# Optimization experiments

Hardware: AMD Instinct MI355X
Metric: run time of the kernel (lower is better)

## Reference

```python
import jax, jax.numpy as jnp
import numpy as np

EPS = 1e-12  # F.normalize eps

def _normalize(v, axis):
    n = jnp.sqrt(jnp.sum(v * v, axis=axis, keepdims=True))
    return v / jnp.maximum(n, EPS)

def setup_inputs() -> dict:
    key = jax.random.key(0)
    ks = jax.random.split(key, 7)
    N, D, E = 100000, 128, 1600000
    x = jax.random.normal(ks[0], (N, D), dtype=jnp.float32)
    edge_index = jax.random.randint(ks[1], (2, E), 0, N, dtype=jnp.int64)
    s = 1.0 / np.sqrt(D)
    W_l = jax.random.normal(ks[2], (D, D), dtype=jnp.float32) * s
    b_l = jnp.zeros((D,), dtype=jnp.float32)
    W_r = jax.random.normal(ks[3], (D, D), dtype=jnp.float32) * s
    W1 = jax.random.normal(ks[4], (D, 10), dtype=jnp.float32)
    W2 = jax.random.normal(ks[5], (D, 20), dtype=jnp.float32)
    return {"x": x, "edge_index": edge_index, "W_l": W_l, "b_l": b_l,
            "W_r": W_r, "W1": W1, "W2": W2}

def reference(x, edge_index, W_l, b_l, W_r, W1, W2):
    N = x.shape[0]
    src, dst = edge_index[0], edge_index[1]
    # SAGEConv mean aggregation: gather source feats, scatter-mean to targets
    msg = x[src]                                   # [E, D]
    agg = jax.ops.segment_sum(msg, dst, num_segments=N)     # [N, D]
    deg = jax.ops.segment_sum(jnp.ones_like(dst, dtype=x.dtype), dst,
                              num_segments=N)               # [N]
    agg = agg / jnp.maximum(deg, 1.0)[:, None]
    # out = lin_l(agg) + lin_r(x)
    h = agg @ W_l + b_l + x @ W_r                  # [N, D]
    # NormedLinear heads: 10 * norm(h, dim=1) @ norm(W, dim=0)
    hn = _normalize(h, axis=1)
    out1 = 10.0 * (hn @ _normalize(W1, axis=0))
    out2 = 10.0 * (hn @ _normalize(W2, axis=0))
    return (out1, out2, h)
```

## Files before the change

kernel.cpp:

```cpp
#include <hip/hip_runtime.h>
#include <math.h>


typedef __attribute__((ext_vector_type(8))) short s16x8;
typedef __attribute__((ext_vector_type(4))) float f32x4;

#define NBLK 128
#define BLKT 512
#define SH 8
#define BMASK 255

static __device__ __forceinline__ unsigned short f2b(float f) {
  unsigned u = __builtin_bit_cast(unsigned, f);
  u += 0x7fff + ((u >> 16) & 1);
  return (unsigned short)(u >> 16);
}
static __device__ __forceinline__ float b2f(unsigned short s) {
  unsigned u = ((unsigned)s) << 16;
  return __builtin_bit_cast(float, u);
}


__global__ __launch_bounds__(BLKT) void radix_hist(
    const int* __restrict__ ei, int* __restrict__ G, int E, int nb, int CH)
{
  __shared__ int cnt[512];
  const int b = blockIdx.x;
  const int t = threadIdx.x;
  for (int i = t; i < 512; i += BLKT) cnt[i] = 0;
  __syncthreads();
  const int e0 = b * CH, e1 = min(E, e0 + CH);
  for (int e = e0 + t; e < e1; e += BLKT)
    atomicAdd(&cnt[ei[(size_t)E + e] >> SH], 1);
  __syncthreads();
  for (int k = t; k < nb; k += BLKT)
    G[(size_t)k * NBLK + b] = cnt[k];
}

#define SCAN_CHUNK 2048

__global__ __launch_bounds__(256) void scan1_kernel(
    const int* __restrict__ cnt, int* __restrict__ offs,
    int* __restrict__ csum, int n)
{
  __shared__ int s_scan[256];
  const int t = threadIdx.x;
  const int base = blockIdx.x * SCAN_CHUNK + t * 8;
  int v[8];
  int s = 0;
#pragma unroll
  for (int k = 0; k < 8; ++k) {
    v[k] = (base + k < n) ? cnt[base + k] : 0;
    s += v[k];
  }
  s_scan[t] = s;
  __syncthreads();
#pragma unroll
  for (int off = 1; off < 256; off <<= 1) {
    int add = (t >= off) ? s_scan[t - off] : 0;
    __syncthreads();
    s_scan[t] += add;
    __syncthreads();
  }
  int run = s_scan[t] - s;
#pragma unroll
  for (int k = 0; k < 8; ++k) {
    if (base + k < n) offs[base + k] = run;
    run += v[k];
  }
  if (t == 255) csum[blockIdx.x] = s_scan[255];
}

__global__ __launch_bounds__(256) void scan2_kernel(int* __restrict__ csum, int nc)
{
  __shared__ int s_scan[256];
  const int t = threadIdx.x;
  int c = (t < nc) ? csum[t] : 0;
  s_scan[t] = c;
  __syncthreads();
#pragma unroll
  for (int off = 1; off < 256; off <<= 1) {
    int add = (t >= off) ? s_scan[t - off] : 0;
    __syncthreads();
    s_scan[t] += add;
    __syncthreads();
  }
  if (t < nc) csum[t] = s_scan[t] - c;
}

__global__ __launch_bounds__(256) void scan3_add(
    int* __restrict__ G, const int* __restrict__ csum, int n)
{
  int i = blockIdx.x * blockDim.x + threadIdx.x;
  if (i < n) G[i] += csum[i / SCAN_CHUNK];
}

__global__ __launch_bounds__(BLKT) void radix_scatter(
    const int* __restrict__ ei, const int* __restrict__ G,
    int* __restrict__ ebuf, int E, int nb, int CH)
{
  __shared__ int cur[512];
  const int b = blockIdx.x;
  const int t = threadIdx.x;
  for (int k = t; k < nb; k += BLKT) cur[k] = G[(size_t)k * NBLK + b];
  __syncthreads();
  const int e0 = b * CH, e1 = min(E, e0 + CH);
  for (int e = e0 + t; e < e1; e += BLKT) {
    int src = ei[e];
    int dst = ei[(size_t)E + e];
    int pos = atomicAdd(&cur[dst >> SH], 1);
    ebuf[pos] = (src << SH) | (dst & BMASK);
  }
}

__global__ __launch_bounds__(256) void csr_finalize(
    const int* __restrict__ G, const int* __restrict__ ebuf,
    int* __restrict__ offs, int* __restrict__ elist, int N, int E, int nb)
{
  __shared__ int cnt[256];
  __shared__ int sc[256];
  __shared__ int cur[256];
  const int b = blockIdx.x;
  const int t = threadIdx.x;
  const int e0 = G[(size_t)b * NBLK];
  const int e1 = (b + 1 < nb) ? G[(size_t)(b + 1) * NBLK] : E;

  cnt[t] = 0;
  __syncthreads();
  for (int j = e0 + t; j < e1; j += 256)
    atomicAdd(&cnt[ebuf[j] & BMASK], 1);
  __syncthreads();
  int v = cnt[t];
  sc[t] = v;
  __syncthreads();
#pragma unroll
  for (int off = 1; off < 256; off <<= 1) {
    int add = (t >= off) ? sc[t - off] : 0;
    __syncthreads();
    sc[t] += add;
    __syncthreads();
  }
  int ex = e0 + sc[t] - v;
  int node = (b << SH) + t;
  if (node < N) offs[node] = ex;
  cur[t] = ex;
  if (b == 0 && t == 0) offs[N] = E;
  __syncthreads();
  for (int j = e0 + t; j < e1; j += 256) {
    int w = ebuf[j];
    int pos = atomicAdd(&cur[w & BMASK], 1);
    elist[pos] = w >> SH;
  }
}


__global__ __launch_bounds__(256) void conv_x_kernel(
    const float* __restrict__ x, short* __restrict__ xb, int n8)
{
  int stride = gridDim.x * blockDim.x;
  for (int i = blockIdx.x * blockDim.x + threadIdx.x; i < n8; i += stride) {
    float4 v0 = ((const float4*)x)[(size_t)i * 2];
    float4 v1 = ((const float4*)x)[(size_t)i * 2 + 1];
    s16x8 o;
    o[0] = (short)f2b(v0.x); o[1] = (short)f2b(v0.y);
    o[2] = (short)f2b(v0.z); o[3] = (short)f2b(v0.w);
    o[4] = (short)f2b(v1.x); o[5] = (short)f2b(v1.y);
    o[6] = (short)f2b(v1.z); o[7] = (short)f2b(v1.w);
    ((s16x8*)xb)[i] = o;
  }
}


__global__ __launch_bounds__(256) void agg_gather_b(
    const short* __restrict__ xb, const int* __restrict__ offs,
    const int* __restrict__ elist, short* __restrict__ aggb, int N)
{
  const int lane = threadIdx.x & 63;
  const int row = blockIdx.x * 4 + (threadIdx.x >> 6);
  if (row >= N) return;
  const int qt = lane >> 4;
  const int c  = lane & 15;
  const int start = offs[row], end = offs[row + 1];
  float a[8] = {0.f, 0.f, 0.f, 0.f, 0.f, 0.f, 0.f, 0.f};
  for (int j = start + qt; j < end; j += 4) {
    const s16x8 v = *(const s16x8*)&xb[(size_t)elist[j] * 128 + c * 8];
#pragma unroll
    for (int k = 0; k < 8; ++k) a[k] += b2f((unsigned short)v[k]);
  }
#pragma unroll
  for (int k = 0; k < 8; ++k) {
    a[k] += __shfl_xor(a[k], 16);
    a[k] += __shfl_xor(a[k], 32);
  }
  if (qt == 0) {
    float rd = 1.0f / fmaxf((float)(end - start), 1.0f);
    s16x8 o;
#pragma unroll
    for (int k = 0; k < 8; ++k) o[k] = (short)f2b(a[k] * rd);
    *(s16x8*)&aggb[(size_t)row * 128 + c * 8] = o;
  }
}

__global__ __launch_bounds__(256) void conv_w_kernel(
    const float* __restrict__ Wl, const float* __restrict__ Wr,
    short* __restrict__ wbT)
{
  int i = blockIdx.x * blockDim.x + threadIdx.x;
  if (i < 128 * 256) {
    int c = i >> 8;
    int k = i & 255;
    float v = (k < 128) ? Wl[(size_t)k * 128 + c] : Wr[(size_t)(k - 128) * 128 + c];
    wbT[i] = (short)f2b(v);
  }
}


__global__ __launch_bounds__(256, 2) void gemm_mfma(
    const short* __restrict__ aggb, const float* __restrict__ x,
    const short* __restrict__ wbT, const float* __restrict__ bl,
    float* __restrict__ h, int N)
{
  __shared__ short A_s[128][72];
  __shared__ short B_s[128][72];

  const int t = threadIdx.x;
  const int lane = t & 63;
  const int wid = t >> 6;
  const int wr = wid >> 1;
  const int wc = wid & 1;
  const int row0 = blockIdx.x * 128;
  const int l15 = lane & 15;
  const int lhi = lane >> 4;

  f32x4 acc[4][4];
#pragma unroll
  for (int m = 0; m < 4; ++m)
#pragma unroll
    for (int n = 0; n < 4; ++n) acc[m][n] = (f32x4){0.f, 0.f, 0.f, 0.f};

  for (int kc = 0; kc < 4; ++kc) {
    __syncthreads();
    const int kbase = (kc & 1) * 64;
#pragma unroll
    for (int uu = 0; uu < 4; ++uu) {
      int u = t + uu * 256;
      int r = u >> 3;
      int s = u & 7;
      s16x8 va = {0, 0, 0, 0, 0, 0, 0, 0};
      int grow = row0 + r;
      if (grow < N) {
        if (kc < 2) {
          va = *(const s16x8*)&aggb[(size_t)grow * 128 + kbase + s * 8];
        } else {
          float4 f0 = ((const float4*)x)[(size_t)grow * 32 + (kc & 1) * 16 + s * 2];
          float4 f1 = ((const float4*)x)[(size_t)grow * 32 + (kc & 1) * 16 + s * 2 + 1];
          va[0] = (short)f2b(f0.x); va[1] = (short)f2b(f0.y);
          va[2] = (short)f2b(f0.z); va[3] = (short)f2b(f0.w);
          va[4] = (short)f2b(f1.x); va[5] = (short)f2b(f1.y);
          va[6] = (short)f2b(f1.z); va[7] = (short)f2b(f1.w);
        }
      }
      *(s16x8*)&A_s[r][s * 8] = va;
      s16x8 vb = *(const s16x8*)&wbT[(size_t)r * 256 + kc * 64 + s * 8];
      *(s16x8*)&B_s[r][s * 8] = vb;
    }
    __syncthreads();

#pragma unroll
    for (int ks = 0; ks < 64; ks += 32) {
      const int klo = ks + lhi * 8;
      s16x8 af[4], bf[4];
#pragma unroll
      for (int m = 0; m < 4; ++m)
        af[m] = *(const s16x8*)&A_s[wr * 64 + m * 16 + l15][klo];
#pragma unroll
      for (int n = 0; n < 4; ++n)
        bf[n] = *(const s16x8*)&B_s[wc * 64 + n * 16 + l15][klo];
#pragma unroll
      for (int m = 0; m < 4; ++m)
#pragma unroll
        for (int n = 0; n < 4; ++n)
          acc[m][n] = __builtin_amdgcn_mfma_f32_16x16x32_bf16(
              af[m], bf[n], acc[m][n], 0, 0, 0);
    }
  }

  float bcol[4];
#pragma unroll
  for (int n = 0; n < 4; ++n) bcol[n] = bl[wc * 64 + n * 16 + l15];
#pragma unroll
  for (int m = 0; m < 4; ++m) {
    int grow_base = row0 + wr * 64 + m * 16 + lhi * 4;
#pragma unroll
    for (int r = 0; r < 4; ++r) {
      int grow = grow_base + r;
      if (grow < N) {
#pragma unroll
        for (int n = 0; n < 4; ++n) {
          int col = wc * 64 + n * 16 + l15;
          h[(size_t)grow * 128 + col] = acc[m][n][r] + bcol[n];
        }
      }
    }
  }
}


__global__ __launch_bounds__(256) void edge_scatter(
    const float* __restrict__ x, const int* __restrict__ ei,
    float* __restrict__ agg, float* __restrict__ deg, int E)
{
  long long total = (long long)E * 32;
  long long stride = (long long)gridDim.x * blockDim.x;
  for (long long i = (long long)blockIdx.x * blockDim.x + threadIdx.x;
       i < total; i += stride) {
    int e = (int)(i >> 5);
    int c = (int)(i & 31);
    int src = ei[e];
    int dst = ei[(size_t)E + e];
    float4 v = ((const float4*)x)[(size_t)src * 32 + c];
    float* a = agg + (size_t)dst * 128 + c * 4;
    atomicAdd(a + 0, v.x);
    atomicAdd(a + 1, v.y);
    atomicAdd(a + 2, v.z);
    atomicAdd(a + 3, v.w);
    if (c == 0) atomicAdd(deg + dst, 1.0f);
  }
}

#define FMA4(accR, wv, s) { accR[0] += (s) * wv.x; accR[1] += (s) * wv.y; \
                            accR[2] += (s) * wv.z; accR[3] += (s) * wv.w; }

__global__ __launch_bounds__(256, 2) void gemm_h(
    const float* __restrict__ x, const float* __restrict__ Wl,
    const float* __restrict__ bl, const float* __restrict__ Wr,
    const float* __restrict__ degf, float* __restrict__ aggh, int N)
{
  __shared__ float a_s[128][36];
  __shared__ float x_s[128][36];
  __shared__ float wl_s[32][128];
  __shared__ float wr_s[32][128];

  const int t = threadIdx.x;
  const int tx = t & 15;
  const int ty = t >> 4;
  const int row0 = blockIdx.x * 128;

  float acc0[8][4];
  float acc1[8][4];
#pragma unroll
  for (int r = 0; r < 8; ++r)
#pragma unroll
    for (int c = 0; c < 4; ++c) { acc0[r][c] = 0.f; acc1[r][c] = 0.f; }

  for (int kc = 0; kc < 4; ++kc) {
    __syncthreads();
#pragma unroll
    for (int j = 0; j < 4; ++j) {
      int i = t + 256 * j;
      int r = i >> 3;
      int c4 = i & 7;
      int row = row0 + r;
      float4 av = {0.f, 0.f, 0.f, 0.f};
      float4 xv = {0.f, 0.f, 0.f, 0.f};
      if (row < N) {
        float rd = 1.0f / fmaxf(degf[row], 1.0f);
        av = ((const float4*)aggh)[(size_t)row * 32 + kc * 8 + c4];
        av.x *= rd; av.y *= rd; av.z *= rd; av.w *= rd;
        xv = ((const float4*)x)[(size_t)row * 32 + kc * 8 + c4];
      }
      *(float4*)&a_s[r][c4 * 4] = av;
      *(float4*)&x_s[r][c4 * 4] = xv;
    }
#pragma unroll
    for (int j = 0; j < 4; ++j) {
      int i = t + 256 * j;
      int kk = i >> 5;
      int c4 = i & 31;
      ((float4*)wl_s[kk])[c4] = ((const float4*)Wl)[(size_t)(kc * 32 + kk) * 32 + c4];
      ((float4*)wr_s[kk])[c4] = ((const float4*)Wr)[(size_t)(kc * 32 + kk) * 32 + c4];
    }
    __syncthreads();

#pragma unroll
    for (int k4 = 0; k4 < 8; ++k4) {
      float4 wl0[4], wl1[4], wr0[4], wr1[4];
#pragma unroll
      for (int kk = 0; kk < 4; ++kk) {
        int k = k4 * 4 + kk;
        wl0[kk] = *(const float4*)&wl_s[k][tx * 4];
        wl1[kk] = *(const float4*)&wl_s[k][64 + tx * 4];
        wr0[kk] = *(const float4*)&wr_s[k][tx * 4];
        wr1[kk] = *(const float4*)&wr_s[k][64 + tx * 4];
      }
#pragma unroll
      for (int r = 0; r < 8; ++r) {
        int rr = ty + 16 * r;
        float4 a  = *(const float4*)&a_s[rr][k4 * 4];
        float4 xv = *(const float4*)&x_s[rr][k4 * 4];
        FMA4(acc0[r], wl0[0], a.x); FMA4(acc0[r], wl0[1], a.y);
        FMA4(acc0[r], wl0[2], a.z); FMA4(acc0[r], wl0[3], a.w);
        FMA4(acc0[r], wr0[0], xv.x); FMA4(acc0[r], wr0[1], xv.y);
        FMA4(acc0[r], wr0[2], xv.z); FMA4(acc0[r], wr0[3], xv.w);
        FMA4(acc1[r], wl1[0], a.x); FMA4(acc1[r], wl1[1], a.y);
        FMA4(acc1[r], wl1[2], a.z); FMA4(acc1[r], wl1[3], a.w);
        FMA4(acc1[r], wr1[0], xv.x); FMA4(acc1[r], wr1[1], xv.y);
        FMA4(acc1[r], wr1[2], xv.z); FMA4(acc1[r], wr1[3], xv.w);
      }
    }
  }

  float4 b0 = ((const float4*)bl)[tx];
  float4 b1 = ((const float4*)bl)[16 + tx];
#pragma unroll
  for (int r = 0; r < 8; ++r) {
    int row = row0 + ty + 16 * r;
    if (row < N) {
      float4 o0 = { acc0[r][0] + b0.x, acc0[r][1] + b0.y,
                    acc0[r][2] + b0.z, acc0[r][3] + b0.w };
      float4 o1 = { acc1[r][0] + b1.x, acc1[r][1] + b1.y,
                    acc1[r][2] + b1.z, acc1[r][3] + b1.w };
      ((float4*)aggh)[(size_t)row * 32 + tx] = o0;
      ((float4*)aggh)[(size_t)row * 32 + 16 + tx] = o1;
    }
  }
}


__global__ __launch_bounds__(256) void head_kernel(
    const float* __restrict__ h, const float* __restrict__ W1,
    const float* __restrict__ W2,
    float* __restrict__ out1, float* __restrict__ out2,
    int N, int c1, int c2)
{
  __shared__ float wc_s[30][132];
  __shared__ float wnorm[30];
  const int nc = c1 + c2;

  for (int i = threadIdx.x; i < nc * 128; i += 256) {
    int j = i >> 7, l = i & 127;
    wc_s[j][l] = (j < c1) ? W1[(size_t)l * c1 + j]
                          : W2[(size_t)l * c2 + (j - c1)];
  }
  __syncthreads();
  if (threadIdx.x < nc) {
    float ss = 0.f;
    for (int l = 0; l < 128; ++l) { float v = wc_s[threadIdx.x][l]; ss += v * v; }
    wnorm[threadIdx.x] = 1.0f / fmaxf(sqrtf(ss), 1e-12f);
  }
  __syncthreads();
  for (int i = threadIdx.x; i < nc * 128; i += 256) {
    int j = i >> 7;
    wc_s[j][i & 127] *= wnorm[j];
  }
  __syncthreads();

  int row = blockIdx.x * 256 + threadIdx.x;
  if (row >= N) return;
  const float4* h4 = (const float4*)(h + (size_t)row * 128);
  float acc[30];
#pragma unroll
  for (int j = 0; j < 30; ++j) acc[j] = 0.f;
  float ss = 0.f;
#pragma unroll 4
  for (int kk = 0; kk < 32; ++kk) {
    float4 v = h4[kk];
    ss += v.x * v.x + v.y * v.y + v.z * v.z + v.w * v.w;
#pragma unroll
    for (int j = 0; j < 30; ++j) {
      const float4 w = *(const float4*)&wc_s[j][kk * 4];
      acc[j] += v.x * w.x + v.y * w.y + v.z * w.z + v.w * w.w;
    }
  }
  float scale = 10.0f / fmaxf(sqrtf(ss), 1e-12f);
#pragma unroll
  for (int j = 0; j < 10; ++j) out1[(size_t)row * 10 + j] = scale * acc[j];
#pragma unroll
  for (int j = 0; j < 20; ++j) out2[(size_t)row * 20 + j] = scale * acc[10 + j];
}


extern "C" void kernel_launch(void* const* d_in, const int* in_sizes, int n_in,
                              void* d_out, int out_size, void* d_ws, size_t ws_size,
                              hipStream_t stream)
{
  const float* x  = (const float*)d_in[0];
  const int*   ei = (const int*)d_in[1];
  const float* Wl = (const float*)d_in[2];
  const float* bl = (const float*)d_in[3];
  const float* Wr = (const float*)d_in[4];
  const float* W1 = (const float*)d_in[5];
  const float* W2 = (const float*)d_in[6];

  const int N  = in_sizes[0] / 128;
  const int E  = in_sizes[1] / 2;
  const int c1 = in_sizes[5] / 128;
  const int c2 = in_sizes[6] / 128;
  const int nb = (N + 255) >> SH;
  const int nbk = nb * NBLK;
  const int CH = (E + NBLK - 1) / NBLK;

  float* out1 = (float*)d_out;
  float* out2 = out1 + (size_t)N * c1;
  float* h    = out2 + (size_t)N * c2;

  size_t ints = (size_t)nbk + 256 + (N + 1) + 2 * (size_t)E;
  ints = (ints + 3) & ~(size_t)3;
  const size_t need = ints * sizeof(int)
                    + ((size_t)N * 128 + 128 * 256) * sizeof(short);

  if (ws_size >= need && nb <= 512) {
    int* G     = (int*)d_ws;
    int* csum  = G + nbk;
    int* offs  = csum + 256;
    int* ebuf  = offs + (N + 1);
    int* elist = ebuf + E;
    short* aggb = (short*)((int*)d_ws + ints);
    short* wbT  = aggb + (size_t)N * 128;
    short* xb   = (short*)h;
    const int nchunks = (nbk + SCAN_CHUNK - 1) / SCAN_CHUNK;

    conv_x_kernel<<<2048, 256, 0, stream>>>(x, xb, N * 16);
    radix_hist<<<NBLK, BLKT, 0, stream>>>(ei, G, E, nb, CH);
    scan1_kernel<<<nchunks, 256, 0, stream>>>(G, G, csum, nbk);
    scan2_kernel<<<1, 256, 0, stream>>>(csum, nchunks);
    scan3_add<<<(nbk + 255) / 256, 256, 0, stream>>>(G, csum, nbk);
    radix_scatter<<<NBLK, BLKT, 0, stream>>>(ei, G, ebuf, E, nb, CH);
    csr_finalize<<<nb, 256, 0, stream>>>(G, ebuf, offs, elist, N, E, nb);
    agg_gather_b<<<(N + 3) / 4, 256, 0, stream>>>(xb, offs, elist, aggb, N);
    conv_w_kernel<<<128, 256, 0, stream>>>(Wl, Wr, wbT);
    gemm_mfma<<<(N + 127) / 128, 256, 0, stream>>>(aggb, x, wbT, bl, h, N);
  } else {
    float* deg = out1;
    hipMemsetAsync(h,   0, (size_t)N * 128 * sizeof(float), stream);
    hipMemsetAsync(deg, 0, (size_t)N * sizeof(float), stream);
    edge_scatter<<<4096, 256, 0, stream>>>(x, ei, h, deg, E);
    gemm_h<<<(N + 127) / 128, 256, 0, stream>>>(x, Wl, bl, Wr, deg, h, N);
  }
  head_kernel<<<(N + 255) / 256, 256, 0, stream>>>(h, W1, W2, out1, out2, N, c1, c2);
}
```

Baseline: 199.4 us.

## Fuse normalized-head projection into MFMA GEMM and stage bf16 x/agg in h buffer

The GEMM epilogue now computes per-row L2 norms and the two normalized-linear heads from an LDS copy of h, which removes the separate head kernel and its re-read of h. Bf16 x and aggregated features are packed side by side in one 256-wide bf16 row inside the h output buffer, so the GEMM reads a single bf16 operand instead of converting fp32 x on the fly. The separate workspace aggb buffer goes away. The risks are higher LDS use (about 68KB per block), which may cut occupancy, and a fast path that now applies only when c1 == 10 and c2 == 20.

```diff
diff --git a/kernel.cpp b/kernel.cpp
--- a/kernel.cpp
+++ b/kernel.cpp
@@ -155,25 +155,26 @@
 
 
 __global__ __launch_bounds__(256) void conv_x_kernel(
-    const float* __restrict__ x, short* __restrict__ xb, int n8)
+    const float* __restrict__ x, short* __restrict__ hs, int n8)
 {
   int stride = gridDim.x * blockDim.x;
   for (int i = blockIdx.x * blockDim.x + threadIdx.x; i < n8; i += stride) {
-    float4 v0 = ((const float4*)x)[(size_t)i * 2];
-    float4 v1 = ((const float4*)x)[(size_t)i * 2 + 1];
+    int row = i >> 4, seg = i & 15;
+    float4 v0 = ((const float4*)x)[(size_t)row * 32 + seg * 2];
+    float4 v1 = ((const float4*)x)[(size_t)row * 32 + seg * 2 + 1];
     s16x8 o;
     o[0] = (short)f2b(v0.x); o[1] = (short)f2b(v0.y);
     o[2] = (short)f2b(v0.z); o[3] = (short)f2b(v0.w);
     o[4] = (short)f2b(v1.x); o[5] = (short)f2b(v1.y);
     o[6] = (short)f2b(v1.z); o[7] = (short)f2b(v1.w);
-    ((s16x8*)xb)[i] = o;
+    *(s16x8*)&hs[(size_t)row * 256 + seg * 8] = o;
   }
 }
 
 
 __global__ __launch_bounds__(256) void agg_gather_b(
-    const short* __restrict__ xb, const int* __restrict__ offs,
-    const int* __restrict__ elist, short* __restrict__ aggb, int N)
+    const short* __restrict__ hs_in, short* __restrict__ hs_out,
+    const int* __restrict__ offs, const int* __restrict__ elist, int N)
 {
   const int lane = threadIdx.x & 63;
   const int row = blockIdx.x * 4 + (threadIdx.x >> 6);
@@ -183,7 +184,7 @@
   const int start = offs[row], end = offs[row + 1];
   float a[8] = {0.f, 0.f, 0.f, 0.f, 0.f, 0.f, 0.f, 0.f};
   for (int j = start + qt; j < end; j += 4) {
-    const s16x8 v = *(const s16x8*)&xb[(size_t)elist[j] * 128 + c * 8];
+    const s16x8 v = *(const s16x8*)&hs_in[(size_t)elist[j] * 256 + c * 8];
 #pragma unroll
     for (int k = 0; k < 8; ++k) a[k] += b2f((unsigned short)v[k]);
   }
@@ -197,7 +198,7 @@
     s16x8 o;
 #pragma unroll
     for (int k = 0; k < 8; ++k) o[k] = (short)f2b(a[k] * rd);
-    *(s16x8*)&aggb[(size_t)row * 128 + c * 8] = o;
+    *(s16x8*)&hs_out[(size_t)row * 256 + 128 + c * 8] = o;
   }
 }
 
@@ -209,19 +210,44 @@
   if (i < 128 * 256) {
     int c = i >> 8;
     int k = i & 255;
-    float v = (k < 128) ? Wl[(size_t)k * 128 + c] : Wr[(size_t)(k - 128) * 128 + c];
+    float v = (k < 128) ? Wr[(size_t)k * 128 + c] : Wl[(size_t)(k - 128) * 128 + c];
     wbT[i] = (short)f2b(v);
   }
 }
 
-
-__global__ __launch_bounds__(256, 2) void gemm_mfma(
-    const short* __restrict__ aggb, const float* __restrict__ x,
-    const short* __restrict__ wbT, const float* __restrict__ bl,
-    float* __restrict__ h, int N)
-{
-  __shared__ short A_s[128][72];
-  __shared__ short B_s[128][72];
+__global__ __launch_bounds__(128) void conv_wcn(
+    const float* __restrict__ W1, const float* __restrict__ W2,
+    float* __restrict__ wcnf, int c1, int c2)
+{
+  int j = blockIdx.x;
+  int l = threadIdx.x;
+  const float* W;
+  int cols, col;
+  if (j < c1) { W = W1; cols = c1; col = j; }
+  else        { W = W2; cols = c2; col = j - c1; }
+  float v = W[(size_t)l * cols + col];
+  float ss = v * v;
+#pragma unroll
+  for (int m = 1; m <= 32; m <<= 1) ss += __shfl_xor(ss, m);
+  __shared__ float sred[2];
+  if ((l & 63) == 0) sred[l >> 6] = ss;
+  __syncthreads();
+  float n = sqrtf(sred[0] + sred[1]);
+  wcnf[(size_t)j * 128 + l] = v / fmaxf(n, 1e-12f);
+}
+
+
+__global__ __launch_bounds__(256, 2) void gemm_fused(
+    const short* __restrict__ hs, const short* __restrict__ wbT,
+    const float* __restrict__ bl, const float* __restrict__ wcnf,
+    float* __restrict__ h, float* __restrict__ out1, float* __restrict__ out2,
+    int N)
+{
+  __shared__ __align__(16) char smem[68608];
+  short (*A_s)[72] = reinterpret_cast<short(*)[72]>(smem);
+  short (*B_s)[72] = reinterpret_cast<short(*)[72]>(smem + 18432);
+  float (*H_s)[132] = reinterpret_cast<float(*)[132]>(smem);
+  float (*rowss)[128] = reinterpret_cast<float(*)[128]>(smem + 67584);
 
   const int t = threadIdx.x;
   const int lane = t & 63;
@@ -240,7 +266,6 @@
 
   for (int kc = 0; kc < 4; ++kc) {
     __syncthreads();
-    const int kbase = (kc & 1) * 64;
 #pragma unroll
     for (int uu = 0; uu < 4; ++uu) {
       int u = t + uu * 256;
@@ -248,18 +273,8 @@
       int s = u & 7;
       s16x8 va = {0, 0, 0, 0, 0, 0, 0, 0};
       int grow = row0 + r;
-      if (grow < N) {
-        if (kc < 2) {
-          va = *(const s16x8*)&aggb[(size_t)grow * 128 + kbase + s * 8];
-        } else {
-          float4 f0 = ((const float4*)x)[(size_t)grow * 32 + (kc & 1) * 16 + s * 2];
-          float4 f1 = ((const float4*)x)[(size_t)grow * 32 + (kc & 1) * 16 + s * 2 + 1];
-          va[0] = (short)f2b(f0.x); va[1] = (short)f2b(f0.y);
-          va[2] = (short)f2b(f0.z); va[3] = (short)f2b(f0.w);
-          va[4] = (short)f2b(f1.x); va[5] = (short)f2b(f1.y);
-          va[6] = (short)f2b(f1.z); va[7] = (short)f2b(f1.w);
-        }
-      }
+      if (grow < N)
+        va = *(const s16x8*)&hs[(size_t)grow * 256 + kc * 64 + s * 8];
       *(s16x8*)&A_s[r][s * 8] = va;
       s16x8 vb = *(const s16x8*)&wbT[(size_t)r * 256 + kc * 64 + s * 8];
       *(s16x8*)&B_s[r][s * 8] = vb;
@@ -285,21 +300,62 @@
     }
   }
 
+  __syncthreads();
+
   float bcol[4];
 #pragma unroll
   for (int n = 0; n < 4; ++n) bcol[n] = bl[wc * 64 + n * 16 + l15];
 #pragma unroll
   for (int m = 0; m < 4; ++m) {
-    int grow_base = row0 + wr * 64 + m * 16 + lhi * 4;
 #pragma unroll
     for (int r = 0; r < 4; ++r) {
-      int grow = grow_base + r;
+      int lr = wr * 64 + m * 16 + lhi * 4 + r;
+      int grow = row0 + lr;
+      float hv[4];
+      float ps = 0.f;
+#pragma unroll
+      for (int n = 0; n < 4; ++n) {
+        hv[n] = acc[m][n][r] + bcol[n];
+        ps += hv[n] * hv[n];
+      }
+#pragma unroll
+      for (int mask = 1; mask < 16; mask <<= 1) ps += __shfl_xor(ps, mask);
       if (grow < N) {
 #pragma unroll
         for (int n = 0; n < 4; ++n) {
           int col = wc * 64 + n * 16 + l15;
-          h[(size_t)grow * 128 + col] = acc[m][n][r] + bcol[n];
+          H_s[lr][col] = hv[n];
+          h[(size_t)grow * 128 + col] = hv[n];
         }
+        if (l15 == 0) rowss[wc][lr] = ps;
+      }
+    }
+  }
+  __syncthreads();
+
+  {
+    int row = t >> 1;
+    int half = t & 1;
+    int grow = row0 + row;
+    if (grow < N) {
+      float sc = 10.0f / fmaxf(sqrtf(rowss[0][row] + rowss[1][row]), 1e-12f);
+      float acch[15];
+#pragma unroll
+      for (int j = 0; j < 15; ++j) acch[j] = 0.f;
+      for (int k = 0; k < 128; k += 4) {
+        float4 hv = *(const float4*)&H_s[row][k];
+#pragma unroll
+        for (int j = 0; j < 15; ++j) {
+          const float4 w = *(const float4*)&wcnf[(size_t)(half * 15 + j) * 128 + k];
+          acch[j] += hv.x * w.x + hv.y * w.y + hv.z * w.z + hv.w * w.w;
+        }
+      }
+#pragma unroll
+      for (int j = 0; j < 15; ++j) {
+        int jj = half * 15 + j;
+        float o = sc * acch[j];
+        if (jj < 10) out1[(size_t)grow * 10 + jj] = o;
+        else         out2[(size_t)grow * 20 + (jj - 10)] = o;
       }
     }
   }
@@ -426,7 +482,6 @@
   }
 }
 
-
 __global__ __launch_bounds__(256) void head_kernel(
     const float* __restrict__ h, const float* __restrict__ W1,
     const float* __restrict__ W2,
@@ -507,35 +562,38 @@
   size_t ints = (size_t)nbk + 256 + (N + 1) + 2 * (size_t)E;
   ints = (ints + 3) & ~(size_t)3;
   const size_t need = ints * sizeof(int)
-                    + ((size_t)N * 128 + 128 * 256) * sizeof(short);
-
-  if (ws_size >= need && nb <= 512) {
+                    + (size_t)128 * 256 * sizeof(short)
+                    + (size_t)30 * 128 * sizeof(float);
+
+  if (ws_size >= need && nb <= 512 && c1 == 10 && c2 == 20) {
     int* G     = (int*)d_ws;
     int* csum  = G + nbk;
     int* offs  = csum + 256;
     int* ebuf  = offs + (N + 1);
     int* elist = ebuf + E;
-    short* aggb = (short*)((int*)d_ws + ints);
-    short* wbT  = aggb + (size_t)N * 128;
-    short* xb   = (short*)h;
+    short* wbT  = (short*)((int*)d_ws + ints);
+    float* wcnf = (float*)(wbT + 128 * 256);
+    short* hs   = (short*)h;
     const int nchunks = (nbk + SCAN_CHUNK - 1) / SCAN_CHUNK;
 
-    conv_x_kernel<<<2048, 256, 0, stream>>>(x, xb, N * 16);
+    conv_x_kernel<<<2048, 256, 0, stream>>>(x, hs, N * 16);
     radix_hist<<<NBLK, BLKT, 0, stream>>>(ei, G, E, nb, CH);
     scan1_kernel<<<nchunks, 256, 0, stream>>>(G, G, csum, nbk);
     scan2_kernel<<<1, 256, 0, stream>>>(csum, nchunks);
     scan3_add<<<(nbk + 255) / 256, 256, 0, stream>>>(G, csum, nbk);
     radix_scatter<<<NBLK, BLKT, 0, stream>>>(ei, G, ebuf, E, nb, CH);
     csr_finalize<<<nb, 256, 0, stream>>>(G, ebuf, offs, elist, N, E, nb);
-    agg_gather_b<<<(N + 3) / 4, 256, 0, stream>>>(xb, offs, elist, aggb, N);
+    agg_gather_b<<<(N + 3) / 4, 256, 0, stream>>>(hs, hs, offs, elist, N);
     conv_w_kernel<<<128, 256, 0, stream>>>(Wl, Wr, wbT);
-    gemm_mfma<<<(N + 127) / 128, 256, 0, stream>>>(aggb, x, wbT, bl, h, N);
+    conv_wcn<<<c1 + c2, 128, 0, stream>>>(W1, W2, wcnf, c1, c2);
+    gemm_fused<<<(N + 127) / 128, 256, 0, stream>>>(
+        hs, wbT, bl, wcnf, h, out1, out2, N);
   } else {
     float* deg = out1;
     hipMemsetAsync(h,   0, (size_t)N * 128 * sizeof(float), stream);
     hipMemsetAsync(deg, 0, (size_t)N * sizeof(float), stream);
     edge_scatter<<<4096, 256, 0, stream>>>(x, ei, h, deg, E);
     gemm_h<<<(N + 127) / 128, 256, 0, stream>>>(x, Wl, bl, Wr, deg, h, N);
-  }
-  head_kernel<<<(N + 255) / 256, 256, 0, stream>>>(h, W1, W2, out1, out2, N, c1, c2);
-}
+    head_kernel<<<(N + 255) / 256, 256, 0, stream>>>(h, W1, W2, out1, out2, N, c1, c2);
+  }
+}
```

New measurement: 269.6 us. 35.2% more time.
